# Kernel optimization log

Measured on AMD Instinct MI355X. Metric: run time of the kernel, lower is better.

Reference implementation:

```python
import jax, jax.numpy as jnp
import numpy as np

N_NODES = 100000
N_EDGES = 3200000
IN_FEATS, N_HIDDEN, OUT_FEATS = 256, 128, 40


def setup_inputs() -> dict:
    key = jax.random.key(0)
    ks = jax.random.split(key, 8)
    x = jax.random.normal(ks[0], (N_NODES, IN_FEATS), dtype=jnp.float32)
    W0 = jax.random.normal(ks[1], (IN_FEATS, N_HIDDEN), dtype=jnp.float32) * (1.0 / np.sqrt(IN_FEATS))
    b0 = jnp.zeros((N_HIDDEN,), dtype=jnp.float32)
    W1 = jax.random.normal(ks[2], (N_HIDDEN, OUT_FEATS), dtype=jnp.float32) * (1.0 / np.sqrt(N_HIDDEN))
    b1 = jnp.zeros((OUT_FEATS,), dtype=jnp.float32)
    edge_weight = jax.random.uniform(ks[3], (N_EDGES,), dtype=jnp.float32)
    src = jax.random.randint(ks[4], (N_EDGES,), 0, N_NODES)
    dst = jax.random.randint(ks[5], (N_EDGES,), 0, N_NODES)
    return {"x": x, "W0": W0, "b0": b0, "W1": W1, "b1": b1,
            "edge_weight": edge_weight, "src": src, "dst": dst}


def reference(x, W0, b0, W1, b1, edge_weight, src, dst):
    n_nodes = x.shape[0]

    def gcn_conv(h, W, b):
        # linear transform first (PyG-style GCNConv), then sparse aggregate (SpMM)
        h = h @ W                                  # [N, d_out]
        msg = h[src] * edge_weight[:, None]        # [E, d_out] gathered + scaled
        agg = jax.ops.segment_sum(msg, dst, num_segments=n_nodes)  # scatter-add
        return agg + b

    h = jax.nn.relu(gcn_conv(x, W0, b0))
    out = gcn_conv(h, W1, b1)
    return jax.nn.log_softmax(out, axis=1)
```

## Files before the change

### kernel.cpp

```cpp
#include <hip/hip_runtime.h>
#include <hip/hip_bf16.h>
#include <cstdint>
#include <cstddef>

#define N_NODES   100000
#define N_EDGES   3200000
#define IN_FEATS  256
#define N_HIDDEN  128
#define OUT_FEATS 40

#define NB        196
#define EPB       8192
#define NBLK      391
#define HIST_M    (NB * NBLK)
#define N_TILES   3125
#define TPB       2
#define G0BLKS    ((N_TILES + TPB - 1) / TPB)

#if defined(__has_builtin)
#  if __has_builtin(__builtin_amdgcn_cvt_pk_f32_fp8) && \
      __has_builtin(__builtin_amdgcn_cvt_pk_fp8_f32)
#    define USE_FP8_H0 1
#  endif
#endif
#ifndef USE_FP8_H0
#  define USE_FP8_H0 0
#endif

typedef __attribute__((ext_vector_type(8))) __bf16 bf16x8;
typedef __attribute__((ext_vector_type(4))) float f32x4;
typedef __attribute__((ext_vector_type(2))) float f32x2;

__device__ __forceinline__ void pkfma(f32x2& a, unsigned int u, f32x2 w2) {
  f32x2 b;
  b.x = __uint_as_float(u << 16);
  b.y = __uint_as_float(u & 0xFFFF0000u);
  a += b * w2;
}

#define ACC8P(A_, V_, W2_)   \
  pkfma(A_[0], (V_).x, W2_); \
  pkfma(A_[1], (V_).y, W2_); \
  pkfma(A_[2], (V_).z, W2_); \
  pkfma(A_[3], (V_).w, W2_);

#if USE_FP8_H0
#define FP8ACC(A_, V_, W2_) {                                          \
  f32x2 d_;                                                            \
  d_ = __builtin_amdgcn_cvt_pk_f32_fp8((V_).x, false); A_[0] += d_ * (W2_); \
  d_ = __builtin_amdgcn_cvt_pk_f32_fp8((V_).x, true ); A_[1] += d_ * (W2_); \
  d_ = __builtin_amdgcn_cvt_pk_f32_fp8((V_).y, false); A_[2] += d_ * (W2_); \
  d_ = __builtin_amdgcn_cvt_pk_f32_fp8((V_).y, true ); A_[3] += d_ * (W2_); \
  d_ = __builtin_amdgcn_cvt_pk_f32_fp8((V_).z, false); A_[4] += d_ * (W2_); \
  d_ = __builtin_amdgcn_cvt_pk_f32_fp8((V_).z, true ); A_[5] += d_ * (W2_); \
  d_ = __builtin_amdgcn_cvt_pk_f32_fp8((V_).w, false); A_[6] += d_ * (W2_); \
  d_ = __builtin_amdgcn_cvt_pk_f32_fp8((V_).w, true ); A_[7] += d_ * (W2_); }
#endif

__device__ __forceinline__ void gemm0_block(
    int bid, const float* __restrict__ x, const uint4* __restrict__ w0f,
    unsigned char* __restrict__ h0) {
  __shared__ __align__(16) unsigned short xb[32 * 264];
  const int tid  = threadIdx.x;
  const int lane = tid & 63;
  const int wave = tid >> 6;
  const int rb   = wave & 1;
  const int ch   = wave >> 1;
  const int l15  = lane & 15;
  const int g    = lane >> 4;

  bf16x8 Bf[4][8];
#pragma unroll
  for (int cb = 0; cb < 4; ++cb)
#pragma unroll
    for (int q = 0; q < 8; ++q)
      Bf[cb][q] = __builtin_bit_cast(bf16x8, w0f[((ch * 4 + cb) * 8 + q) * 64 + lane]);

  for (int t = 0; t < TPB; ++t) {
    const int tile = bid * TPB + t;
    if (tile >= N_TILES) break;
    const int row0 = tile * 32;
    __syncthreads();
    for (int i = tid; i < 32 * 128; i += 256) {
      const int row = i >> 7, kp = i & 127;
      const float2 v = *(const float2*)(x + (size_t)(row0 + row) * IN_FEATS + kp * 2);
      __hip_bfloat162 p;
      p.x = __float2bfloat16(v.x);
      p.y = __float2bfloat16(v.y);
      *(unsigned int*)&xb[row * 264 + kp * 2] = *(unsigned int*)&p;
    }
    __syncthreads();

    f32x4 acc[4];
#pragma unroll
    for (int cb = 0; cb < 4; ++cb) acc[cb] = (f32x4){0.f, 0.f, 0.f, 0.f};

#pragma unroll
    for (int q = 0; q < 8; ++q) {
      const bf16x8 a = *(const bf16x8*)&xb[(rb * 16 + l15) * 264 + q * 32 + g * 8];
      acc[0] = __builtin_amdgcn_mfma_f32_16x16x32_bf16(a, Bf[0][q], acc[0], 0, 0, 0);
      acc[1] = __builtin_amdgcn_mfma_f32_16x16x32_bf16(a, Bf[1][q], acc[1], 0, 0, 0);
      acc[2] = __builtin_amdgcn_mfma_f32_16x16x32_bf16(a, Bf[2][q], acc[2], 0, 0, 0);
      acc[3] = __builtin_amdgcn_mfma_f32_16x16x32_bf16(a, Bf[3][q], acc[3], 0, 0, 0);
    }

#pragma unroll
    for (int cb = 0; cb < 4; ++cb) {
      const int col = ch * 64 + cb * 16 + l15;
#pragma unroll
      for (int r = 0; r < 4; ++r) {
        const int row = row0 + rb * 16 + g * 4 + r;
#if USE_FP8_H0
        const int pk = __builtin_amdgcn_cvt_pk_fp8_f32(acc[cb][r], acc[cb][r], 0, false);
        h0[(size_t)row * N_HIDDEN + col] = (unsigned char)(pk & 0xFF);
#else
        __hip_bfloat16 hb = __float2bfloat16(acc[cb][r]);
        ((unsigned short*)h0)[(size_t)row * N_HIDDEN + col] = *(unsigned short*)&hb;
#endif
      }
    }
  }
}

__device__ __forceinline__ void bucket_scan_block(
    int b, const int* __restrict__ bsum, int* __restrict__ histG) {
  __shared__ int sh[256];
  __shared__ int pr[256];
  const int t = threadIdx.x;

  sh[t] = (t < b) ? bsum[t] : 0;
  __syncthreads();
#pragma unroll
  for (int off = 128; off > 0; off >>= 1) {
    if (t < off) sh[t] += sh[t + off];
    __syncthreads();
  }
  const int base = sh[0];

  const int row = b * NBLK;
  const int i0 = 2 * t, i1 = 2 * t + 1;
  int a = 0, c = 0;
  if (t < 196) {
    a = histG[row + i0];
    if (i1 < NBLK) c = histG[row + i1];
  }
  pr[t] = a + c;
  __syncthreads();
  for (int off = 1; off < 256; off <<= 1) {
    int v = (t >= off) ? pr[t - off] : 0;
    __syncthreads();
    pr[t] += v;
    __syncthreads();
  }
  if (t < 196) {
    const int ebase = (t > 0) ? pr[t - 1] : 0;
    histG[row + i0] = base + ebase;
    if (i1 < NBLK) histG[row + i1] = base + ebase + a;
  }
}

__global__ __launch_bounds__(256) void bscan_gemm0_kernel(
    const int* __restrict__ bsum, int* __restrict__ histG,
    const float* __restrict__ x, const uint4* __restrict__ w0f,
    unsigned char* __restrict__ h0) {
  if (blockIdx.x < NB) bucket_scan_block(blockIdx.x, bsum, histG);
  else                 gemm0_block(blockIdx.x - NB, x, w0f, h0);
}

__global__ __launch_bounds__(256) void p1hist_kernel(
    const int* __restrict__ dst, int* __restrict__ histG,
    const float* __restrict__ W1, uint4* __restrict__ w1f,
    const float* __restrict__ W0, uint4* __restrict__ w0f,
    int* __restrict__ bsum) {
  const int tid = threadIdx.x;
  const int blk = blockIdx.x;

  if (blk >= NBLK) {
    if (blk == NBLK) {
      for (int t = tid; t < 3 * 4 * 64; t += 256) {
        const int ln  = t & 63;
        const int qq  = (t >> 6) & 3;
        const int nt  = t >> 8;
        const int l15 = ln & 15;
        const int gg  = ln >> 4;
        const int c   = nt * 16 + l15;
        const int k0  = qq * 32 + gg * 8;
        uint4 u;
        __hip_bfloat162 p;
#define W1AT(i_) ((c < OUT_FEATS) ? W1[(size_t)(k0 + (i_)) * OUT_FEATS + c] : 0.f)
        p.x = __float2bfloat16(W1AT(0)); p.y = __float2bfloat16(W1AT(1));
        u.x = *(unsigned int*)&p;
        p.x = __float2bfloat16(W1AT(2)); p.y = __float2bfloat16(W1AT(3));
        u.y = *(unsigned int*)&p;
        p.x = __float2bfloat16(W1AT(4)); p.y = __float2bfloat16(W1AT(5));
        u.z = *(unsigned int*)&p;
        p.x = __float2bfloat16(W1AT(6)); p.y = __float2bfloat16(W1AT(7));
        u.w = *(unsigned int*)&p;
#undef W1AT
        w1f[t] = u;
      }
    } else {
      const int pb = blk - NBLK - 1;
      for (int fi = pb * 512 + tid; fi < pb * 512 + 512; fi += 256) {
        const int ln  = fi & 63;
        const int qq  = (fi >> 6) & 7;
        const int ct  = fi >> 9;
        const int col = ct * 16 + (ln & 15);
        const int k0  = qq * 32 + (ln >> 4) * 8;
        uint4 u;
        __hip_bfloat162 p;
        p.x = __float2bfloat16(W0[(size_t)(k0 + 0) * N_HIDDEN + col]);
        p.y = __float2bfloat16(W0[(size_t)(k0 + 1) * N_HIDDEN + col]);
        u.x = *(unsigned int*)&p;
        p.x = __float2bfloat16(W0[(size_t)(k0 + 2) * N_HIDDEN + col]);
        p.y = __float2bfloat16(W0[(size_t)(k0 + 3) * N_HIDDEN + col]);
        u.y = *(unsigned int*)&p;
        p.x = __float2bfloat16(W0[(size_t)(k0 + 4) * N_HIDDEN + col]);
        p.y = __float2bfloat16(W0[(size_t)(k0 + 5) * N_HIDDEN + col]);
        u.z = *(unsigned int*)&p;
        p.x = __float2bfloat16(W0[(size_t)(k0 + 6) * N_HIDDEN + col]);
        p.y = __float2bfloat16(W0[(size_t)(k0 + 7) * N_HIDDEN + col]);
        u.w = *(unsigned int*)&p;
        w0f[fi] = u;
      }
    }
    return;
  }

  __shared__ int lh[NB];
  for (int i = tid; i < NB; i += 256) lh[i] = 0;
  __syncthreads();

  const int e0 = blk * EPB;
  const int e1 = min(e0 + EPB, N_EDGES);
  for (int i = e0 + tid; i < e1; i += 256)
    atomicAdd(&lh[dst[i] >> 9], 1);
  __syncthreads();

  for (int i = tid; i < NB; i += 256) {
    histG[i * NBLK + blk] = lh[i];
    atomicAdd(&bsum[i], lh[i]);
  }
}

__global__ __launch_bounds__(256) void p1scatter_kernel(
    const int* __restrict__ src, const int* __restrict__ dst,
    const float* __restrict__ ew, const int* __restrict__ histG,
    uint2* __restrict__ bucketed) {
  __shared__ uint2 stage[EPB];
  __shared__ unsigned char sbkt[EPB];
  __shared__ int lcnt[NB];
  __shared__ int lbase[NB];
  __shared__ int spart[256];
  const int tid = threadIdx.x;
  const int blk = blockIdx.x;
  const int e0 = blk * EPB;
  const int e1 = min(e0 + EPB, N_EDGES);

  for (int i = tid; i < NB; i += 256) lcnt[i] = 0;
  __syncthreads();

  for (int i = e0 + tid; i < e1; i += 256)
    atomicAdd(&lcnt[dst[i] >> 9], 1);
  __syncthreads();

  const int myv = (tid < NB) ? lcnt[tid] : 0;
  spart[tid] = myv;
  __syncthreads();
  for (int off = 1; off < 256; off <<= 1) {
    int u = (tid >= off) ? spart[tid - off] : 0;
    __syncthreads();
    spart[tid] += u;
    __syncthreads();
  }
  if (tid < NB) { lbase[tid] = spart[tid] - myv; lcnt[tid] = spart[tid] - myv; }
  __syncthreads();

  for (int i = e0 + tid; i < e1; i += 256) {
    const int d = dst[i];
    const int b = d >> 9;
    const int pos = atomicAdd(&lcnt[b], 1);
    stage[pos] = make_uint2((unsigned)src[i] | ((unsigned)(d & 511) << 17),
                            __float_as_uint(ew[i]));
    sbkt[pos] = (unsigned char)b;
  }
  __syncthreads();

  const int n = e1 - e0;
  for (int i = tid; i < n; i += 256) {
    const int b = sbkt[i];
    const int gpos = histG[b * NBLK + blk] + (i - lbase[b]);
    bucketed[gpos] = stage[i];
  }
}

__global__ __launch_bounds__(256) void p2place_kernel(
    const uint2* __restrict__ bucketed, const int* __restrict__ histG,
    int* __restrict__ offsets, int2* __restrict__ srcw) {
  __shared__ int cnt[512];
  __shared__ int part[256];
  const int t = threadIdx.x;
  const int b = blockIdx.x;
  const int node0 = b << 9;
  const int beg = histG[b * NBLK];
  const int end = (b == NB - 1) ? N_EDGES : histG[(b + 1) * NBLK];

  cnt[t] = 0; cnt[t + 256] = 0;
  __syncthreads();

  for (int j = beg + t; j < end; j += 256)
    atomicAdd(&cnt[bucketed[j].x >> 17], 1);
  __syncthreads();

  const int a0 = cnt[2 * t];
  const int a1 = cnt[2 * t + 1];
  part[t] = a0 + a1;
  __syncthreads();
  for (int off = 1; off < 256; off <<= 1) {
    int v = (t >= off) ? part[t - off] : 0;
    __syncthreads();
    part[t] += v;
    __syncthreads();
  }
  const int base = (t > 0) ? part[t - 1] : 0;

  const int o0 = beg + base;
  const int o1 = o0 + a0;
  cnt[2 * t]     = o0;
  cnt[2 * t + 1] = o1;
  const int n0 = node0 + 2 * t;
  if (n0 < N_NODES)     offsets[n0]     = o0;
  if (n0 + 1 < N_NODES) offsets[n0 + 1] = o1;
  if (b == NB - 1 && t == 0) offsets[N_NODES] = N_EDGES;
  __syncthreads();

  for (int j = beg + t; j < end; j += 256) {
    const uint2 en = bucketed[j];
    const int slot = atomicAdd(&cnt[en.x >> 17], 1);
    srcw[slot] = make_int2((int)(en.x & 0x1FFFFu), (int)en.y);
  }
}

#if USE_FP8_H0
__global__ __launch_bounds__(256) void gather0_gemm1_kernel(
    const uint4* __restrict__ h0q, const int2* __restrict__ srcw,
    const int* __restrict__ offsets, const float* __restrict__ b0,
    const uint4* __restrict__ w1f, unsigned short* __restrict__ h1b) {
  __shared__ float hs[4][132];
  const int wave = threadIdx.x >> 6;
  const int lane = threadIdx.x & 63;
  const int node = blockIdx.x * 4 + wave;
  const int g  = lane >> 3;
  const int fl = lane & 7;

  const int beg = __builtin_amdgcn_readfirstlane(offsets[node]);
  const int end = __builtin_amdgcn_readfirstlane(offsets[node + 1]);

  f32x2 acc[8];
#pragma unroll
  for (int i = 0; i < 8; ++i) acc[i] = (f32x2){0.f, 0.f};

  if (end > beg) {
    const int e1 = end - 1;
    int2 sa = srcw[min(beg + g, e1)];
    int2 sb = srcw[min(beg + 8 + g, e1)];
    for (int j = beg; j < end; j += 16) {
      const float wa = (j + g < end)     ? __int_as_float(sa.y) : 0.f;
      const float wb = (j + 8 + g < end) ? __int_as_float(sb.y) : 0.f;
      const uint4 va = h0q[(size_t)(unsigned)sa.x * 8 + fl];
      const uint4 vb = h0q[(size_t)(unsigned)sb.x * 8 + fl];
      const int jn = j + 16;
      if (jn < end) {
        sa = srcw[min(jn + g, e1)];
        sb = srcw[min(jn + 8 + g, e1)];
      }
      const f32x2 pa = {wa, wa};
      const f32x2 pb = {wb, wb};
      FP8ACC(acc, va, pa)
      FP8ACC(acc, vb, pb)
    }
  }

#pragma unroll
  for (int i = 0; i < 8; ++i) {
    acc[i].x += __shfl_xor(acc[i].x, 8);
    acc[i].x += __shfl_xor(acc[i].x, 16);
    acc[i].x += __shfl_xor(acc[i].x, 32);
    acc[i].y += __shfl_xor(acc[i].y, 8);
    acc[i].y += __shfl_xor(acc[i].y, 16);
    acc[i].y += __shfl_xor(acc[i].y, 32);
  }

  if (g == 0) {
    const int f0 = fl * 16;
#pragma unroll
    for (int jj = 0; jj < 4; ++jj) {
      const float v0 = acc[2 * jj].x     + b0[f0 + 4 * jj + 0];
      const float v1 = acc[2 * jj].y     + b0[f0 + 4 * jj + 1];
      const float v2 = acc[2 * jj + 1].x + b0[f0 + 4 * jj + 2];
      const float v3 = acc[2 * jj + 1].y + b0[f0 + 4 * jj + 3];
      *(float4*)&hs[wave][f0 + 4 * jj] = make_float4(
          v0 > 0.f ? v0 : 0.f, v1 > 0.f ? v1 : 0.f,
          v2 > 0.f ? v2 : 0.f, v3 > 0.f ? v3 : 0.f);
    }
  }
  __syncthreads();

  const int l15 = lane & 15;
  const int gg  = lane >> 4;
  if (wave < 3) {
    f32x4 c = {0.f, 0.f, 0.f, 0.f};
#pragma unroll
    for (int qq = 0; qq < 4; ++qq) {
      uint4 ua = make_uint4(0, 0, 0, 0);
      if (l15 < 4) {
        const float* hrow = &hs[l15][qq * 32 + gg * 8];
        __hip_bfloat162 p;
        p.x = __float2bfloat16(hrow[0]); p.y = __float2bfloat16(hrow[1]);
        ua.x = *(unsigned int*)&p;
        p.x = __float2bfloat16(hrow[2]); p.y = __float2bfloat16(hrow[3]);
        ua.y = *(unsigned int*)&p;
        p.x = __float2bfloat16(hrow[4]); p.y = __float2bfloat16(hrow[5]);
        ua.z = *(unsigned int*)&p;
        p.x = __float2bfloat16(hrow[6]); p.y = __float2bfloat16(hrow[7]);
        ua.w = *(unsigned int*)&p;
      }
      const uint4 ub = w1f[(wave * 4 + qq) * 64 + lane];
      c = __builtin_amdgcn_mfma_f32_16x16x32_bf16(
            __builtin_bit_cast(bf16x8, ua), __builtin_bit_cast(bf16x8, ub),
            c, 0, 0, 0);
    }
    if (gg == 0) {
#pragma unroll
      for (int r = 0; r < 4; ++r) {
        const int nodeR = blockIdx.x * 4 + r;
        const int f = wave * 16 + l15;
        __hip_bfloat16 hb = __float2bfloat16(c[r]);
        h1b[(size_t)nodeR * 64 + f] = *(unsigned short*)&hb;
      }
    }
  } else {
    if (gg == 0) {
#pragma unroll
      for (int r = 0; r < 4; ++r) {
        const int nodeR = blockIdx.x * 4 + r;
        h1b[(size_t)nodeR * 64 + 48 + l15] = 0;
      }
    }
  }
}
#else
__global__ __launch_bounds__(256) void gather0_gemm1_kernel(
    const uint4* __restrict__ h0q, const int2* __restrict__ srcw,
    const int* __restrict__ offsets, const float* __restrict__ b0,
    const uint4* __restrict__ w1f, unsigned short* __restrict__ h1b) {
  __shared__ float hs[4][132];
  const int wave = threadIdx.x >> 6;
  const int lane = threadIdx.x & 63;
  const int node = blockIdx.x * 4 + wave;
  const int q    = lane >> 4;
  const int fl   = lane & 15;

  const int beg = __builtin_amdgcn_readfirstlane(offsets[node]);
  const int end = __builtin_amdgcn_readfirstlane(offsets[node + 1]);

  f32x2 acc[4];
#pragma unroll
  for (int i = 0; i < 4; ++i) acc[i] = (f32x2){0.f, 0.f};

  if (end > beg) {
    const int e1 = end - 1;
    int2 sa = srcw[min(beg + q, e1)];
    int2 sb = srcw[min(beg + 4 + q, e1)];
    int2 sc = srcw[min(beg + 8 + q, e1)];
    int2 sd = srcw[min(beg + 12 + q, e1)];
    for (int j = beg; j < end; j += 16) {
      const float wa = (j + q < end)      ? __int_as_float(sa.y) : 0.f;
      const float wb = (j + 4 + q < end)  ? __int_as_float(sb.y) : 0.f;
      const float wc = (j + 8 + q < end)  ? __int_as_float(sc.y) : 0.f;
      const float wd = (j + 12 + q < end) ? __int_as_float(sd.y) : 0.f;
      const uint4 va = h0q[(size_t)(unsigned)sa.x * 16 + fl];
      const uint4 vb = h0q[(size_t)(unsigned)sb.x * 16 + fl];
      const uint4 vc = h0q[(size_t)(unsigned)sc.x * 16 + fl];
      const uint4 vd = h0q[(size_t)(unsigned)sd.x * 16 + fl];
      const int jn = j + 16;
      if (jn < end) {
        sa = srcw[min(jn + q, e1)];
        sb = srcw[min(jn + 4 + q, e1)];
        sc = srcw[min(jn + 8 + q, e1)];
        sd = srcw[min(jn + 12 + q, e1)];
      }
      const f32x2 pa = {wa, wa};
      const f32x2 pb = {wb, wb};
      const f32x2 pc = {wc, wc};
      const f32x2 pd = {wd, wd};
      ACC8P(acc, va, pa)
      ACC8P(acc, vb, pb)
      ACC8P(acc, vc, pc)
      ACC8P(acc, vd, pd)
    }
  }

#pragma unroll
  for (int i = 0; i < 4; ++i) {
    acc[i].x += __shfl_xor(acc[i].x, 16);
    acc[i].x += __shfl_xor(acc[i].x, 32);
    acc[i].y += __shfl_xor(acc[i].y, 16);
    acc[i].y += __shfl_xor(acc[i].y, 32);
  }

  if (q == 0) {
    const int f0 = fl * 8;
    float t[8];
#pragma unroll
    for (int i = 0; i < 8; ++i) {
      const float a = ((i & 1) ? acc[i >> 1].y : acc[i >> 1].x);
      const float v = a + b0[f0 + i];
      t[i] = v > 0.f ? v : 0.f;
    }
    *(float4*)&hs[wave][f0]     = make_float4(t[0], t[1], t[2], t[3]);
    *(float4*)&hs[wave][f0 + 4] = make_float4(t[4], t[5], t[6], t[7]);
  }
  __syncthreads();

  const int l15 = lane & 15;
  const int gg  = lane >> 4;
  if (wave < 3) {
    f32x4 c = {0.f, 0.f, 0.f, 0.f};
#pragma unroll
    for (int qq = 0; qq < 4; ++qq) {
      uint4 ua = make_uint4(0, 0, 0, 0);
      if (l15 < 4) {
        const float* hrow = &hs[l15][qq * 32 + gg * 8];
        __hip_bfloat162 p;
        p.x = __float2bfloat16(hrow[0]); p.y = __float2bfloat16(hrow[1]);
        ua.x = *(unsigned int*)&p;
        p.x = __float2bfloat16(hrow[2]); p.y = __float2bfloat16(hrow[3]);
        ua.y = *(unsigned int*)&p;
        p.x = __float2bfloat16(hrow[4]); p.y = __float2bfloat16(hrow[5]);
        ua.z = *(unsigned int*)&p;
        p.x = __float2bfloat16(hrow[6]); p.y = __float2bfloat16(hrow[7]);
        ua.w = *(unsigned int*)&p;
      }
      const uint4 ub = w1f[(wave * 4 + qq) * 64 + lane];
      c = __builtin_amdgcn_mfma_f32_16x16x32_bf16(
            __builtin_bit_cast(bf16x8, ua), __builtin_bit_cast(bf16x8, ub),
            c, 0, 0, 0);
    }
    if (gg == 0) {
#pragma unroll
      for (int r = 0; r < 4; ++r) {
        const int nodeR = blockIdx.x * 4 + r;
        const int f = wave * 16 + l15;
        __hip_bfloat16 hb = __float2bfloat16(c[r]);
        h1b[(size_t)nodeR * 64 + f] = *(unsigned short*)&hb;
      }
    }
  } else {
    if (gg == 0) {
#pragma unroll
      for (int r = 0; r < 4; ++r) {
        const int nodeR = blockIdx.x * 4 + r;
        h1b[(size_t)nodeR * 64 + 48 + l15] = 0;
      }
    }
  }
}
#endif

__global__ __launch_bounds__(256) void gather1_lsm_kernel(
    const uint4* __restrict__ h1q, const int2* __restrict__ srcw,
    const int* __restrict__ offsets, const float* __restrict__ b1,
    float* __restrict__ out) {
  const int wave = threadIdx.x >> 6;
  const int lane = threadIdx.x & 63;
  const int node = blockIdx.x * 4 + wave;
  const int g  = lane >> 3;
  const int fl = lane & 7;

  const int beg = __builtin_amdgcn_readfirstlane(offsets[node]);
  const int end = __builtin_amdgcn_readfirstlane(offsets[node + 1]);

  f32x2 acc[4];
#pragma unroll
  for (int i = 0; i < 4; ++i) acc[i] = (f32x2){0.f, 0.f};

  if (end > beg) {
    const int e1 = end - 1;
    int2 sa = srcw[min(beg + g, e1)];
    int2 sb = srcw[min(beg + 8 + g, e1)];
    int2 sc = srcw[min(beg + 16 + g, e1)];
    int2 sd = srcw[min(beg + 24 + g, e1)];
    for (int j = beg; j < end; j += 32) {
      const float wa = (j + g < end)      ? __int_as_float(sa.y) : 0.f;
      const float wb = (j + 8 + g < end)  ? __int_as_float(sb.y) : 0.f;
      const float wc = (j + 16 + g < end) ? __int_as_float(sc.y) : 0.f;
      const float wd = (j + 24 + g < end) ? __int_as_float(sd.y) : 0.f;
      const uint4 va = h1q[(size_t)(unsigned)sa.x * 8 + fl];
      const uint4 vb = h1q[(size_t)(unsigned)sb.x * 8 + fl];
      const uint4 vc = h1q[(size_t)(unsigned)sc.x * 8 + fl];
      const uint4 vd = h1q[(size_t)(unsigned)sd.x * 8 + fl];
      const int jn = j + 32;
      if (jn < end) {
        sa = srcw[min(jn + g, e1)];
        sb = srcw[min(jn + 8 + g, e1)];
        sc = srcw[min(jn + 16 + g, e1)];
        sd = srcw[min(jn + 24 + g, e1)];
      }
      const f32x2 pa = {wa, wa};
      const f32x2 pb = {wb, wb};
      const f32x2 pc = {wc, wc};
      const f32x2 pd = {wd, wd};
      ACC8P(acc, va, pa)
      ACC8P(acc, vb, pb)
      ACC8P(acc, vc, pc)
      ACC8P(acc, vd, pd)
    }
  }

  float o[8];
#pragma unroll
  for (int i = 0; i < 4; ++i) {
    float x0 = acc[i].x, y0 = acc[i].y;
    x0 += __shfl_xor(x0, 8); x0 += __shfl_xor(x0, 16); x0 += __shfl_xor(x0, 32);
    y0 += __shfl_xor(y0, 8); y0 += __shfl_xor(y0, 16); y0 += __shfl_xor(y0, 32);
    o[2 * i] = x0; o[2 * i + 1] = y0;
  }

  const bool valid = (fl < 5);
  float m = -INFINITY;
  if (valid) {
    const int f0 = fl * 8;
#pragma unroll
    for (int i = 0; i < 8; ++i) {
      o[i] += b1[f0 + i];
      m = fmaxf(m, o[i]);
    }
  }
  m = fmaxf(m, __shfl_xor(m, 1));
  m = fmaxf(m, __shfl_xor(m, 2));
  m = fmaxf(m, __shfl_xor(m, 4));

  float s = 0.f;
  if (valid) {
#pragma unroll
    for (int i = 0; i < 8; ++i) s += expf(o[i] - m);
  }
  s += __shfl_xor(s, 1);
  s += __shfl_xor(s, 2);
  s += __shfl_xor(s, 4);

  if (lane < 5) {
    const float lse = m + logf(s);
    float* op = out + (size_t)node * OUT_FEATS + fl * 8;
    *(float4*)op       = make_float4(o[0] - lse, o[1] - lse,
                                     o[2] - lse, o[3] - lse);
    *(float4*)(op + 4) = make_float4(o[4] - lse, o[5] - lse,
                                     o[6] - lse, o[7] - lse);
  }
}

extern "C" void kernel_launch(void* const* d_in, const int* in_sizes, int n_in,
                              void* d_out, int out_size, void* d_ws, size_t ws_size,
                              hipStream_t stream) {
  const float* x   = (const float*)d_in[0];
  const float* W0  = (const float*)d_in[1];
  const float* b0  = (const float*)d_in[2];
  const float* W1  = (const float*)d_in[3];
  const float* b1  = (const float*)d_in[4];
  const float* ew  = (const float*)d_in[5];
  const int*   src = (const int*)d_in[6];
  const int*   dst = (const int*)d_in[7];
  float* out = (float*)d_out;

  char* ws = (char*)d_ws;
  unsigned char* h0 = (unsigned char*)(ws);
  int2*  srcw     = (int2*)(ws + 25600000);
  uint2* bucketed = (uint2*)(ws + 51200000);
  int*   offsets  = (int*)(ws + 76800000);
  int*   histG    = (int*)(ws + 77200064);
  unsigned short* h1b = (unsigned short*)(ws + 77506624);
  uint4* w1f      = (uint4*)(ws + 90306624);
  uint4* w0f      = (uint4*)(ws + 90318912);
  int*   bsum     = (int*)(ws + 90384448);

  hipMemsetAsync(bsum, 0, NB * sizeof(int), stream);
  p1hist_kernel<<<NBLK + 9, 256, 0, stream>>>(dst, histG, W1, w1f, W0, w0f, bsum);
  bscan_gemm0_kernel<<<NB + G0BLKS, 256, 0, stream>>>(
      bsum, histG, x, w0f, h0);
  p1scatter_kernel<<<NBLK, 256, 0, stream>>>(src, dst, ew, histG, bucketed);
  p2place_kernel<<<NB, 256, 0, stream>>>(bucketed, histG, offsets, srcw);

  gather0_gemm1_kernel<<<N_NODES / 4, 256, 0, stream>>>(
      (const uint4*)h0, srcw, offsets, b0, (const uint4*)w1f, h1b);
  gather1_lsm_kernel<<<N_NODES / 4, 256, 0, stream>>>(
      (const uint4*)h1b, srcw, offsets, b1, out);
}
```

Measured before the change: 475.6 us.

## Split h1 into 32+8 feature arrays and co-schedule gemm0 with place kernel

```diff
diff --git a/kernel.cpp b/kernel.cpp
--- a/kernel.cpp
+++ b/kernel.cpp
@@ -159,12 +159,9 @@
   }
 }
 
-__global__ __launch_bounds__(256) void bscan_gemm0_kernel(
-    const int* __restrict__ bsum, int* __restrict__ histG,
-    const float* __restrict__ x, const uint4* __restrict__ w0f,
-    unsigned char* __restrict__ h0) {
-  if (blockIdx.x < NB) bucket_scan_block(blockIdx.x, bsum, histG);
-  else                 gemm0_block(blockIdx.x - NB, x, w0f, h0);
+__global__ __launch_bounds__(256) void bscan_kernel(
+    const int* __restrict__ bsum, int* __restrict__ histG) {
+  bucket_scan_block(blockIdx.x, bsum, histG);
 }
 
 __global__ __launch_bounds__(256) void p1hist_kernel(
@@ -294,13 +291,12 @@
   }
 }
 
-__global__ __launch_bounds__(256) void p2place_kernel(
-    const uint2* __restrict__ bucketed, const int* __restrict__ histG,
+__device__ __forceinline__ void p2place_block(
+    int b, const uint2* __restrict__ bucketed, const int* __restrict__ histG,
     int* __restrict__ offsets, int2* __restrict__ srcw) {
   __shared__ int cnt[512];
   __shared__ int part[256];
   const int t = threadIdx.x;
-  const int b = blockIdx.x;
   const int node0 = b << 9;
   const int beg = histG[b * NBLK];
   const int end = (b == NB - 1) ? N_EDGES : histG[(b + 1) * NBLK];
@@ -341,11 +337,21 @@
   }
 }
 
+__global__ __launch_bounds__(256) void place_gemm0_kernel(
+    const uint2* __restrict__ bucketed, const int* __restrict__ histG,
+    int* __restrict__ offsets, int2* __restrict__ srcw,
+    const float* __restrict__ x, const uint4* __restrict__ w0f,
+    unsigned char* __restrict__ h0) {
+  if (blockIdx.x < NB) p2place_block(blockIdx.x, bucketed, histG, offsets, srcw);
+  else                 gemm0_block(blockIdx.x - NB, x, w0f, h0);
+}
+
 #if USE_FP8_H0
 __global__ __launch_bounds__(256) void gather0_gemm1_kernel(
     const uint4* __restrict__ h0q, const int2* __restrict__ srcw,
     const int* __restrict__ offsets, const float* __restrict__ b0,
-    const uint4* __restrict__ w1f, unsigned short* __restrict__ h1b) {
+    const uint4* __restrict__ w1f, unsigned short* __restrict__ h1a,
+    unsigned short* __restrict__ h1c) {
   __shared__ float hs[4][132];
   const int wave = threadIdx.x >> 6;
   const int lane = threadIdx.x & 63;
@@ -436,15 +442,9 @@
         const int nodeR = blockIdx.x * 4 + r;
         const int f = wave * 16 + l15;
         __hip_bfloat16 hb = __float2bfloat16(c[r]);
-        h1b[(size_t)nodeR * 64 + f] = *(unsigned short*)&hb;
-      }
-    }
-  } else {
-    if (gg == 0) {
-#pragma unroll
-      for (int r = 0; r < 4; ++r) {
-        const int nodeR = blockIdx.x * 4 + r;
-        h1b[(size_t)nodeR * 64 + 48 + l15] = 0;
+        const unsigned short v16 = *(unsigned short*)&hb;
+        if (f < 32)              h1a[(size_t)nodeR * 32 + f] = v16;
+        else if (f < OUT_FEATS)  h1c[(size_t)nodeR * 8 + (f - 32)] = v16;
       }
     }
   }
@@ -453,7 +453,8 @@
 __global__ __launch_bounds__(256) void gather0_gemm1_kernel(
     const uint4* __restrict__ h0q, const int2* __restrict__ srcw,
     const int* __restrict__ offsets, const float* __restrict__ b0,
-    const uint4* __restrict__ w1f, unsigned short* __restrict__ h1b) {
+    const uint4* __restrict__ w1f, unsigned short* __restrict__ h1a,
+    unsigned short* __restrict__ h1c) {
   __shared__ float hs[4][132];
   const int wave = threadIdx.x >> 6;
   const int lane = threadIdx.x & 63;
@@ -553,15 +554,9 @@
         const int nodeR = blockIdx.x * 4 + r;
         const int f = wave * 16 + l15;
         __hip_bfloat16 hb = __float2bfloat16(c[r]);
-        h1b[(size_t)nodeR * 64 + f] = *(unsigned short*)&hb;
-      }
-    }
-  } else {
-    if (gg == 0) {
-#pragma unroll
-      for (int r = 0; r < 4; ++r) {
-        const int nodeR = blockIdx.x * 4 + r;
-        h1b[(size_t)nodeR * 64 + 48 + l15] = 0;
+        const unsigned short v16 = *(unsigned short*)&hb;
+        if (f < 32)              h1a[(size_t)nodeR * 32 + f] = v16;
+        else if (f < OUT_FEATS)  h1c[(size_t)nodeR * 8 + (f - 32)] = v16;
       }
     }
   }
@@ -569,94 +564,96 @@
 #endif
 
 __global__ __launch_bounds__(256) void gather1_lsm_kernel(
-    const uint4* __restrict__ h1q, const int2* __restrict__ srcw,
-    const int* __restrict__ offsets, const float* __restrict__ b1,
-    float* __restrict__ out) {
+    const uint4* __restrict__ h1aq, const unsigned int* __restrict__ h1cd,
+    const int2* __restrict__ srcw, const int* __restrict__ offsets,
+    const float* __restrict__ b1, float* __restrict__ out) {
   const int wave = threadIdx.x >> 6;
   const int lane = threadIdx.x & 63;
   const int node = blockIdx.x * 4 + wave;
-  const int g  = lane >> 3;
-  const int fl = lane & 7;
+  const int g  = lane >> 2;
+  const int fl = lane & 3;
 
   const int beg = __builtin_amdgcn_readfirstlane(offsets[node]);
   const int end = __builtin_amdgcn_readfirstlane(offsets[node + 1]);
 
   f32x2 acc[4];
+  f32x2 accc = {0.f, 0.f};
 #pragma unroll
   for (int i = 0; i < 4; ++i) acc[i] = (f32x2){0.f, 0.f};
 
   if (end > beg) {
     const int e1 = end - 1;
     int2 sa = srcw[min(beg + g, e1)];
-    int2 sb = srcw[min(beg + 8 + g, e1)];
-    int2 sc = srcw[min(beg + 16 + g, e1)];
-    int2 sd = srcw[min(beg + 24 + g, e1)];
+    int2 sb = srcw[min(beg + 16 + g, e1)];
     for (int j = beg; j < end; j += 32) {
       const float wa = (j + g < end)      ? __int_as_float(sa.y) : 0.f;
-      const float wb = (j + 8 + g < end)  ? __int_as_float(sb.y) : 0.f;
-      const float wc = (j + 16 + g < end) ? __int_as_float(sc.y) : 0.f;
-      const float wd = (j + 24 + g < end) ? __int_as_float(sd.y) : 0.f;
-      const uint4 va = h1q[(size_t)(unsigned)sa.x * 8 + fl];
-      const uint4 vb = h1q[(size_t)(unsigned)sb.x * 8 + fl];
-      const uint4 vc = h1q[(size_t)(unsigned)sc.x * 8 + fl];
-      const uint4 vd = h1q[(size_t)(unsigned)sd.x * 8 + fl];
+      const float wb = (j + 16 + g < end) ? __int_as_float(sb.y) : 0.f;
+      const uint4 va = h1aq[(size_t)(unsigned)sa.x * 4 + fl];
+      const uint4 vb = h1aq[(size_t)(unsigned)sb.x * 4 + fl];
+      const unsigned int ca = h1cd[(size_t)(unsigned)sa.x * 4 + fl];
+      const unsigned int cb = h1cd[(size_t)(unsigned)sb.x * 4 + fl];
       const int jn = j + 32;
       if (jn < end) {
         sa = srcw[min(jn + g, e1)];
-        sb = srcw[min(jn + 8 + g, e1)];
-        sc = srcw[min(jn + 16 + g, e1)];
-        sd = srcw[min(jn + 24 + g, e1)];
+        sb = srcw[min(jn + 16 + g, e1)];
       }
       const f32x2 pa = {wa, wa};
       const f32x2 pb = {wb, wb};
-      const f32x2 pc = {wc, wc};
-      const f32x2 pd = {wd, wd};
       ACC8P(acc, va, pa)
+      pkfma(accc, ca, pa);
       ACC8P(acc, vb, pb)
-      ACC8P(acc, vc, pc)
-      ACC8P(acc, vd, pd)
-    }
-  }
-
-  float o[8];
+      pkfma(accc, cb, pb);
+    }
+  }
+
+  float o[8], oc0, oc1;
 #pragma unroll
   for (int i = 0; i < 4; ++i) {
     float x0 = acc[i].x, y0 = acc[i].y;
-    x0 += __shfl_xor(x0, 8); x0 += __shfl_xor(x0, 16); x0 += __shfl_xor(x0, 32);
-    y0 += __shfl_xor(y0, 8); y0 += __shfl_xor(y0, 16); y0 += __shfl_xor(y0, 32);
+    x0 += __shfl_xor(x0, 4); x0 += __shfl_xor(x0, 8);
+    x0 += __shfl_xor(x0, 16); x0 += __shfl_xor(x0, 32);
+    y0 += __shfl_xor(y0, 4); y0 += __shfl_xor(y0, 8);
+    y0 += __shfl_xor(y0, 16); y0 += __shfl_xor(y0, 32);
     o[2 * i] = x0; o[2 * i + 1] = y0;
   }
-
-  const bool valid = (fl < 5);
+  {
+    float x0 = accc.x, y0 = accc.y;
+    x0 += __shfl_xor(x0, 4); x0 += __shfl_xor(x0, 8);
+    x0 += __shfl_xor(x0, 16); x0 += __shfl_xor(x0, 32);
+    y0 += __shfl_xor(y0, 4); y0 += __shfl_xor(y0, 8);
+    y0 += __shfl_xor(y0, 16); y0 += __shfl_xor(y0, 32);
+    oc0 = x0; oc1 = y0;
+  }
+
+  const int f0 = fl * 8;
   float m = -INFINITY;
-  if (valid) {
-    const int f0 = fl * 8;
-#pragma unroll
-    for (int i = 0; i < 8; ++i) {
-      o[i] += b1[f0 + i];
-      m = fmaxf(m, o[i]);
-    }
-  }
+#pragma unroll
+  for (int i = 0; i < 8; ++i) {
+    o[i] += b1[f0 + i];
+    m = fmaxf(m, o[i]);
+  }
+  oc0 += b1[32 + 2 * fl];
+  oc1 += b1[33 + 2 * fl];
+  m = fmaxf(m, oc0);
+  m = fmaxf(m, oc1);
   m = fmaxf(m, __shfl_xor(m, 1));
   m = fmaxf(m, __shfl_xor(m, 2));
-  m = fmaxf(m, __shfl_xor(m, 4));
 
   float s = 0.f;
-  if (valid) {
-#pragma unroll
-    for (int i = 0; i < 8; ++i) s += expf(o[i] - m);
-  }
+#pragma unroll
+  for (int i = 0; i < 8; ++i) s += expf(o[i] - m);
+  s += expf(oc0 - m) + expf(oc1 - m);
   s += __shfl_xor(s, 1);
   s += __shfl_xor(s, 2);
-  s += __shfl_xor(s, 4);
-
-  if (lane < 5) {
+
+  if (lane < 4) {
     const float lse = m + logf(s);
-    float* op = out + (size_t)node * OUT_FEATS + fl * 8;
-    *(float4*)op       = make_float4(o[0] - lse, o[1] - lse,
-                                     o[2] - lse, o[3] - lse);
-    *(float4*)(op + 4) = make_float4(o[4] - lse, o[5] - lse,
-                                     o[6] - lse, o[7] - lse);
+    float* op = out + (size_t)node * OUT_FEATS;
+    *(float4*)(op + f0)     = make_float4(o[0] - lse, o[1] - lse,
+                                          o[2] - lse, o[3] - lse);
+    *(float4*)(op + f0 + 4) = make_float4(o[4] - lse, o[5] - lse,
+                                          o[6] - lse, o[7] - lse);
+    *(float2*)(op + 32 + 2 * fl) = make_float2(oc0 - lse, oc1 - lse);
   }
 }
 
@@ -679,20 +676,20 @@
   uint2* bucketed = (uint2*)(ws + 51200000);
   int*   offsets  = (int*)(ws + 76800000);
   int*   histG    = (int*)(ws + 77200064);
-  unsigned short* h1b = (unsigned short*)(ws + 77506624);
-  uint4* w1f      = (uint4*)(ws + 90306624);
-  uint4* w0f      = (uint4*)(ws + 90318912);
-  int*   bsum     = (int*)(ws + 90384448);
+  unsigned short* h1a = (unsigned short*)(ws + 77506624);
+  unsigned short* h1c = (unsigned short*)(ws + 83906624);
+  uint4* w1f      = (uint4*)(ws + 85506624);
+  uint4* w0f      = (uint4*)(ws + 85518912);
+  int*   bsum     = (int*)(ws + 85584448);
 
   hipMemsetAsync(bsum, 0, NB * sizeof(int), stream);
   p1hist_kernel<<<NBLK + 9, 256, 0, stream>>>(dst, histG, W1, w1f, W0, w0f, bsum);
-  bscan_gemm0_kernel<<<NB + G0BLKS, 256, 0, stream>>>(
-      bsum, histG, x, w0f, h0);
+  bscan_kernel<<<NB, 256, 0, stream>>>(bsum, histG);
   p1scatter_kernel<<<NBLK, 256, 0, stream>>>(src, dst, ew, histG, bucketed);
-  p2place_kernel<<<NB, 256, 0, stream>>>(bucketed, histG, offsets, srcw);
-
+  place_gemm0_kernel<<<NB + G0BLKS, 256, 0, stream>>>(
+      bucketed, histG, offsets, srcw, x, w0f, h0);
   gather0_gemm1_kernel<<<N_NODES / 4, 256, 0, stream>>>(
-      (const uint4*)h0, srcw, offsets, b0, (const uint4*)w1f, h1b);
+      (const uint4*)h0, srcw, offsets, b0, (const uint4*)w1f, h1a, h1c);
   gather1_lsm_kernel<<<N_NODES / 4, 256, 0, stream>>>(
-      (const uint4*)h1b, srcw, offsets, b1, out);
-}
+      (const uint4*)h1a, (const unsigned int*)h1c, srcw, offsets, b1, out);
+}
```

Result: faster. 443.4 us (-6.8%).
